# Optimization experiments

Hardware: AMD Instinct MI355X
Metric: run time of the kernel (lower is better)

Reference implementation:

```python
import jax, jax.numpy as jnp
import numpy as np

BETA = 50.0  # params['beta'] threshold for memory update
MEMORY_LEN = 4096


def setup_inputs() -> dict:
    key = jax.random.key(0)
    ks = jax.random.split(key, 7)
    B, D_IN, D_OUT, M = 256, 128, 256, MEMORY_LEN
    return {
        "x": jax.random.normal(ks[0], (B, D_IN), dtype=jnp.float32),
        "mean": jax.random.normal(ks[1], (D_IN,), dtype=jnp.float32),
        "std": jax.random.uniform(ks[2], (D_IN,), dtype=jnp.float32),
        "W1": jax.random.normal(ks[3], (D_IN, D_OUT), dtype=jnp.float32) * 0.1,
        "b1": jax.random.normal(ks[4], (D_OUT,), dtype=jnp.float32) * 0.1,
        "memory": jax.random.normal(ks[5], (M, D_OUT), dtype=jnp.float32),
        "mem_data": jax.random.normal(ks[6], (M, D_IN), dtype=jnp.float32),
    }


def reference(x, mean, std, W1, b1, memory, mem_data):
    # normalize, zeroing columns where std == 0 (as in torch forward)
    zero_std = std == 0
    denom = jnp.where(zero_std, 1.0, std)
    new = jnp.where(zero_std[None, :], 0.0, (x - mean) / denom)  # [B, D_in]

    # encoder: Linear + Tanh
    enc = jnp.tanh(new @ W1 + b1)  # [B, D_out]

    # L1 cdist against full memory (count == memory_len, steady state) + row min
    dist = jnp.abs(enc[:, None, :] - memory[None, :, :]).sum(-1)  # [B, M]
    loss = dist.min(axis=1)  # [B]

    # sequential per-row circular-buffer scatter update (side effect in torch)
    M = memory.shape[0]

    def step(carry, inp):
        mem, md, count = carry
        l, e, xi = inp
        cond = jnp.isfinite(l) & (l <= BETA)
        pos = jnp.mod(count, M)
        mem = mem.at[pos].set(jnp.where(cond, e, mem[pos]))
        md = md.at[pos].set(jnp.where(cond, xi, md[pos]))
        return (mem, md, count + cond.astype(jnp.int32)), None

    # count starts at memory_len (memory full), so writes wrap from position 0
    (mem_out, md_out, _), _ = jax.lax.scan(
        step, (memory, mem_data, jnp.int32(M)), (loss, enc, x)
    )
    return loss, mem_out, md_out
```

## Files before the change

### kernel.cpp

```cpp
#include <hip/hip_runtime.h>
#include <hip/hip_bf16.h>
#include <math.h>

#define B_ROWS 256
#define D_IN   128
#define D_OUT  256
#define M_LEN  4096
#define BETA   50.0f

#define OFF_MEM  (B_ROWS)
#define OFF_MD   (B_ROWS + M_LEN * D_OUT)

__global__ __launch_bounds__(256) void k_prep(
    const float* __restrict__ x, const float* __restrict__ mean,
    const float* __restrict__ stdv, const float* __restrict__ W1,
    const float* __restrict__ b1, float* __restrict__ enc,
    float* __restrict__ out) {
  __shared__ float sx[D_IN];
  const int b = blockIdx.x, j = threadIdx.x;
  if (j < D_IN) {
    float s = stdv[j];
    sx[j] = (s == 0.0f) ? 0.0f : (x[b * D_IN + j] - mean[j]) / s;
  }
  __syncthreads();
  float acc = b1[j];
#pragma unroll 8
  for (int k = 0; k < D_IN; ++k) acc = fmaf(sx[k], W1[k * D_OUT + j], acc);
  enc[b * D_OUT + j] = tanhf(acc);
  if (b == 0) ((unsigned int*)out)[j] = 0x7F800000u;
}

#define TB 32
#define TM 64

__global__ __launch_bounds__(256) void k_dist(
    const float* __restrict__ enc, const float* __restrict__ mem,
    const float4* __restrict__ mem4, const float4* __restrict__ md4,
    float* __restrict__ out) {
  __shared__ __align__(16) float sE[4][32][TB];
  __shared__ __align__(16) float sM[4][32][TM];

  const int t  = threadIdx.x;
  const int w  = t >> 6;
  const int l  = t & 63;
  const int ro = l >> 3;
  const int q  = l & 7;
  const int m0 = blockIdx.x * TM;
  const int b0 = blockIdx.y * TB;
  const int bid = blockIdx.y * 64 + blockIdx.x;

  const float* encp = enc + (b0 + ro) * D_OUT + w * 64 + q * 4;
  const float* memp = mem + (m0 + ro) * D_OUT + w * 64 + q * 4;

  float4 rE[4], rM[8], rE2[4], rM2[8];
  float acc[4][8] = {};

  auto store_lds = [&](const float4* e, const float4* m) {
#pragma unroll
    for (int i = 0; i < 4; ++i) {
      const int row = (i * 8 + ro) ^ (q * 4);
      sE[w][q * 4 + 0][row] = e[i].x;
      sE[w][q * 4 + 1][row] = e[i].y;
      sE[w][q * 4 + 2][row] = e[i].z;
      sE[w][q * 4 + 3][row] = e[i].w;
    }
#pragma unroll
    for (int i = 0; i < 8; ++i) {
      const int row = (i * 8 + ro) ^ (q * 4);
      sM[w][q * 4 + 0][row] = m[i].x;
      sM[w][q * 4 + 1][row] = m[i].y;
      sM[w][q * 4 + 2][row] = m[i].z;
      sM[w][q * 4 + 3][row] = m[i].w;
    }
  };

  auto compute = [&]() {
#pragma unroll
    for (int kk = 0; kk < 32; ++kk) {
      const int sw = (kk >> 2) * 4;
      float4 a   = *(const float4*)&sE[w][kk][(ro * 4) ^ sw];
      float4 bv1 = *(const float4*)&sM[w][kk][(q * 8) ^ sw];
      float4 bv2 = *(const float4*)&sM[w][kk][(q * 8 + 4) ^ sw];
      float av[4] = {a.x, a.y, a.z, a.w};
      float bw[8] = {bv1.x, bv1.y, bv1.z, bv1.w, bv2.x, bv2.y, bv2.z, bv2.w};
#pragma unroll
      for (int i = 0; i < 4; ++i)
#pragma unroll
        for (int j = 0; j < 8; ++j)
          acc[i][j] += fabsf(av[i] - bw[j]);
    }
  };

#pragma unroll
  for (int i = 0; i < 4; ++i) rE[i] = *(const float4*)(encp + i * 8 * D_OUT);
#pragma unroll
  for (int i = 0; i < 8; ++i) rM[i] = *(const float4*)(memp + i * 8 * D_OUT);
  store_lds(rE, rM);

#pragma unroll
  for (int i = 0; i < 4; ++i) rE2[i] = *(const float4*)(encp + 32 + i * 8 * D_OUT);
#pragma unroll
  for (int i = 0; i < 8; ++i) rM2[i] = *(const float4*)(memp + 32 + i * 8 * D_OUT);

  float4 cm0 = mem4[bid * 512 + t];
  float4 cm1 = mem4[bid * 512 + 256 + t];
  float4 cd0 = md4[bid * 256 + t];

  compute();
  store_lds(rE2, rM2);
  compute();

  float* sf = &sM[0][0][0];
#pragma unroll
  for (int i = 0; i < 4; ++i)
#pragma unroll
    for (int j = 0; j < 8; ++j) {
      const int p = i * 8 + j;
      sf[w * 2048 + l * 32 + (p ^ (l & 31))] = acc[i][j];
    }
  __syncthreads();

  {
    const int r = t >> 3, cg = t & 7;
    const int lv = (r >> 2) * 8 + cg;
    float dmin = 3.4e38f;
#pragma unroll
    for (int j = 0; j < 8; ++j) {
      const int p = (r & 3) * 8 + j;
      float s = sf[0 * 2048 + lv * 32 + (p ^ (lv & 31))];
      s += sf[1 * 2048 + lv * 32 + (p ^ (lv & 31))];
      s += sf[2 * 2048 + lv * 32 + (p ^ (lv & 31))];
      s += sf[3 * 2048 + lv * 32 + (p ^ (lv & 31))];
      dmin = fminf(dmin, s);
    }
    dmin = fminf(dmin, __shfl_xor(dmin, 1));
    dmin = fminf(dmin, __shfl_xor(dmin, 2));
    dmin = fminf(dmin, __shfl_xor(dmin, 4));
    if (cg == 0)
      atomicMin((unsigned int*)out + (b0 + r), __float_as_uint(dmin));
  }

  float4* mo = (float4*)(out + OFF_MEM);
  float4* dd = (float4*)(out + OFF_MD);
  mo[bid * 512 + t] = cm0;
  mo[bid * 512 + 256 + t] = cm1;
  dd[bid * 256 + t] = cd0;
}

__global__ __launch_bounds__(256) void k_scatter(float* __restrict__ out,
                                                 const float* __restrict__ enc,
                                                 const float* __restrict__ x) {
  __shared__ int wcount[4];
  int t = threadIdx.x;
  float l = out[t];
  bool cond = isfinite(l) && (l <= BETA);
  unsigned long long m = __ballot(cond);
  int lane = t & 63;
  int wv   = t >> 6;
  int pre_in_wave = __popcll(m & ((1ull << lane) - 1ull));
  if (lane == 0) wcount[wv] = (int)__popcll(m);
  __syncthreads();
  int base = 0;
  for (int w = 0; w < wv; ++w) base += wcount[w];
  if (cond) {
    int pos = base + pre_in_wave;
    float* mrow = out + OFF_MEM + pos * D_OUT;
    const float* erow = enc + t * D_OUT;
    for (int d = 0; d < D_OUT; ++d) mrow[d] = erow[d];
    float* drow = out + OFF_MD + pos * D_IN;
    const float* xrow = x + t * D_IN;
    for (int d = 0; d < D_IN; ++d) drow[d] = xrow[d];
  }
}

extern "C" void kernel_launch(void* const* d_in, const int* in_sizes, int n_in,
                              void* d_out, int out_size, void* d_ws, size_t ws_size,
                              hipStream_t stream) {
  const float* x      = (const float*)d_in[0];
  const float* mean   = (const float*)d_in[1];
  const float* stdv   = (const float*)d_in[2];
  const float* W1     = (const float*)d_in[3];
  const float* b1     = (const float*)d_in[4];
  const float* memory = (const float*)d_in[5];
  const float* memdat = (const float*)d_in[6];
  float* out = (float*)d_out;
  float* enc = (float*)d_ws;

  k_prep<<<dim3(B_ROWS), dim3(256), 0, stream>>>(x, mean, stdv, W1, b1, enc, out);

  k_dist<<<dim3(M_LEN / TM, B_ROWS / TB), dim3(256), 0, stream>>>(
      enc, memory, (const float4*)memory, (const float4*)memdat, out);

  k_scatter<<<dim3(1), dim3(256), 0, stream>>>(out, enc, x);
}
```

Measured before the change: 27.31 us.

## Fuse scatter into distance kernel via last-block completion counter

Removes the separate single-block scatter kernel launch. The last distance block to finish, found with an atomic counter in workspace that the prep kernel resets, runs the ballot/prefix-sum scatter. The change also reduces compute loop unrolling from full to 8. It adds a threadfence and atomic per block, and the scatter copy still runs serially per thread inside one block.

```diff
diff --git a/kernel.cpp b/kernel.cpp
--- a/kernel.cpp
+++ b/kernel.cpp
@@ -11,12 +11,16 @@
 #define OFF_MEM  (B_ROWS)
 #define OFF_MD   (B_ROWS + M_LEN * D_OUT)
 
+#define ENC_F   0
+#define FLAG_F  65536
+
 __global__ __launch_bounds__(256) void k_prep(
     const float* __restrict__ x, const float* __restrict__ mean,
     const float* __restrict__ stdv, const float* __restrict__ W1,
-    const float* __restrict__ b1, float* __restrict__ enc,
+    const float* __restrict__ b1, float* __restrict__ ws,
     float* __restrict__ out) {
   __shared__ float sx[D_IN];
+  float* enc = ws + ENC_F;
   const int b = blockIdx.x, j = threadIdx.x;
   if (j < D_IN) {
     float s = stdv[j];
@@ -28,17 +32,23 @@
   for (int k = 0; k < D_IN; ++k) acc = fmaf(sx[k], W1[k * D_OUT + j], acc);
   enc[b * D_OUT + j] = tanhf(acc);
   if (b == 0) ((unsigned int*)out)[j] = 0x7F800000u;
+  if (b == 0 && j == 0) ((int*)(ws + FLAG_F))[0] = 0;
 }
 
 #define TB 32
 #define TM 64
 
 __global__ __launch_bounds__(256) void k_dist(
-    const float* __restrict__ enc, const float* __restrict__ mem,
+    const float* __restrict__ x, const float* __restrict__ mem,
     const float4* __restrict__ mem4, const float4* __restrict__ md4,
-    float* __restrict__ out) {
+    float* __restrict__ ws, float* __restrict__ out) {
   __shared__ __align__(16) float sE[4][32][TB];
   __shared__ __align__(16) float sM[4][32][TM];
+  __shared__ int wcount[4];
+  __shared__ int slast;
+
+  float* enc = ws + ENC_F;
+  int*   don = (int*)(ws + FLAG_F);
 
   const int t  = threadIdx.x;
   const int w  = t >> 6;
@@ -75,7 +85,7 @@
   };
 
   auto compute = [&]() {
-#pragma unroll
+#pragma unroll 8
     for (int kk = 0; kk < 32; ++kk) {
       const int sw = (kk >> 2) * 4;
       float4 a   = *(const float4*)&sE[w][kk][(ro * 4) ^ sw];
@@ -145,31 +155,39 @@
   mo[bid * 512 + t] = cm0;
   mo[bid * 512 + 256 + t] = cm1;
   dd[bid * 256 + t] = cd0;
-}
-
-__global__ __launch_bounds__(256) void k_scatter(float* __restrict__ out,
-                                                 const float* __restrict__ enc,
-                                                 const float* __restrict__ x) {
-  __shared__ int wcount[4];
-  int t = threadIdx.x;
-  float l = out[t];
-  bool cond = isfinite(l) && (l <= BETA);
-  unsigned long long m = __ballot(cond);
-  int lane = t & 63;
-  int wv   = t >> 6;
-  int pre_in_wave = __popcll(m & ((1ull << lane) - 1ull));
-  if (lane == 0) wcount[wv] = (int)__popcll(m);
-  __syncthreads();
-  int base = 0;
-  for (int w = 0; w < wv; ++w) base += wcount[w];
-  if (cond) {
-    int pos = base + pre_in_wave;
-    float* mrow = out + OFF_MEM + pos * D_OUT;
-    const float* erow = enc + t * D_OUT;
-    for (int d = 0; d < D_OUT; ++d) mrow[d] = erow[d];
-    float* drow = out + OFF_MD + pos * D_IN;
-    const float* xrow = x + t * D_IN;
-    for (int d = 0; d < D_IN; ++d) drow[d] = xrow[d];
+
+  __threadfence();
+  __syncthreads();
+  if (t == 0) {
+    int old = __hip_atomic_fetch_add(don, 1, __ATOMIC_ACQ_REL,
+                                     __HIP_MEMORY_SCOPE_AGENT);
+    slast = (old == 511) ? 1 : 0;
+  }
+  __syncthreads();
+  if (!slast) return;
+
+  {
+    unsigned int lu = __hip_atomic_load((unsigned int*)out + t,
+                                        __ATOMIC_RELAXED,
+                                        __HIP_MEMORY_SCOPE_AGENT);
+    float mn = __uint_as_float(lu);
+    bool cond = isfinite(mn) && (mn <= BETA);
+    unsigned long long bm = __ballot(cond);
+    int lane = t & 63, wv = t >> 6;
+    int pre = __popcll(bm & ((1ull << lane) - 1ull));
+    if (lane == 0) wcount[wv] = (int)__popcll(bm);
+    __syncthreads();
+    int base = 0;
+    for (int wj = 0; wj < wv; ++wj) base += wcount[wj];
+    if (cond) {
+      int pos = base + pre;
+      float* mrow = out + OFF_MEM + pos * D_OUT;
+      const float* erow = enc + t * D_OUT;
+      for (int d = 0; d < D_OUT; ++d) mrow[d] = erow[d];
+      float* drow = out + OFF_MD + pos * D_IN;
+      const float* xrow = x + t * D_IN;
+      for (int d = 0; d < D_IN; ++d) drow[d] = xrow[d];
+    }
   }
 }
 
@@ -184,12 +202,10 @@
   const float* memory = (const float*)d_in[5];
   const float* memdat = (const float*)d_in[6];
   float* out = (float*)d_out;
-  float* enc = (float*)d_ws;
-
-  k_prep<<<dim3(B_ROWS), dim3(256), 0, stream>>>(x, mean, stdv, W1, b1, enc, out);
+  float* ws  = (float*)d_ws;
+
+  k_prep<<<dim3(B_ROWS), dim3(256), 0, stream>>>(x, mean, stdv, W1, b1, ws, out);
 
   k_dist<<<dim3(M_LEN / TM, B_ROWS / TB), dim3(256), 0, stream>>>(
-      enc, memory, (const float4*)memory, (const float4*)memdat, out);
-
-  k_scatter<<<dim3(1), dim3(256), 0, stream>>>(out, enc, x);
+      x, memory, (const float4*)memory, (const float4*)memdat, ws, out);
 }
```

Result: slower. 80.33 us (+194.1%).

## Enlarge distance tile to 64x64 with 8x8 per-thread register blocking

Applied to the files above, without the earlier changes.

The L1 distance kernel tile grows from 32 batch rows x 64 memory rows to 64x64. Each thread now accumulates an 8x8 block instead of 4x8, which raises arithmetic per LDS load and halves the number of times memory rows are reloaded across the batch dimension. The grid shrinks to 256 blocks, and each block copies twice as much memory/mem_data into the output. The costs are higher register pressure (64 accumulators), a larger LDS footprint, and fewer blocks to spread across CUs.

```diff
diff --git a/kernel.cpp b/kernel.cpp
--- a/kernel.cpp
+++ b/kernel.cpp
@@ -30,121 +30,123 @@
   if (b == 0) ((unsigned int*)out)[j] = 0x7F800000u;
 }
 
-#define TB 32
-#define TM 64
-
 __global__ __launch_bounds__(256) void k_dist(
     const float* __restrict__ enc, const float* __restrict__ mem,
     const float4* __restrict__ mem4, const float4* __restrict__ md4,
     float* __restrict__ out) {
-  __shared__ __align__(16) float sE[4][32][TB];
-  __shared__ __align__(16) float sM[4][32][TM];
+  __shared__ __align__(16) float sf[16384];
 
   const int t  = threadIdx.x;
   const int w  = t >> 6;
   const int l  = t & 63;
-  const int ro = l >> 3;
-  const int q  = l & 7;
-  const int m0 = blockIdx.x * TM;
-  const int b0 = blockIdx.y * TB;
+  const int lr = l >> 3;
+  const int lk = l & 7;
+  const int m0 = blockIdx.x * 64;
+  const int b0 = blockIdx.y * 64;
   const int bid = blockIdx.y * 64 + blockIdx.x;
 
-  const float* encp = enc + (b0 + ro) * D_OUT + w * 64 + q * 4;
-  const float* memp = mem + (m0 + ro) * D_OUT + w * 64 + q * 4;
+  const int eb = w * 4096;
+  const int mb = w * 4096 + 2048;
 
-  float4 rE[4], rM[8], rE2[4], rM2[8];
-  float acc[4][8] = {};
+  float acc[8][8] = {};
+  float4 gE[8], gM[8];
 
-  auto store_lds = [&](const float4* e, const float4* m) {
-#pragma unroll
-    for (int i = 0; i < 4; ++i) {
-      const int row = (i * 8 + ro) ^ (q * 4);
-      sE[w][q * 4 + 0][row] = e[i].x;
-      sE[w][q * 4 + 1][row] = e[i].y;
-      sE[w][q * 4 + 2][row] = e[i].z;
-      sE[w][q * 4 + 3][row] = e[i].w;
-    }
-#pragma unroll
-    for (int i = 0; i < 8; ++i) {
-      const int row = (i * 8 + ro) ^ (q * 4);
-      sM[w][q * 4 + 0][row] = m[i].x;
-      sM[w][q * 4 + 1][row] = m[i].y;
-      sM[w][q * 4 + 2][row] = m[i].z;
-      sM[w][q * 4 + 3][row] = m[i].w;
-    }
-  };
+  const float* ep = enc + (b0 + lr) * D_OUT + 64 * w + lk * 4;
+  const float* mp = mem + (m0 + lr) * D_OUT + 64 * w + lk * 4;
 
-  auto compute = [&]() {
-#pragma unroll
-    for (int kk = 0; kk < 32; ++kk) {
-      const int sw = (kk >> 2) * 4;
-      float4 a   = *(const float4*)&sE[w][kk][(ro * 4) ^ sw];
-      float4 bv1 = *(const float4*)&sM[w][kk][(q * 8) ^ sw];
-      float4 bv2 = *(const float4*)&sM[w][kk][(q * 8 + 4) ^ sw];
-      float av[4] = {a.x, a.y, a.z, a.w};
-      float bw[8] = {bv1.x, bv1.y, bv1.z, bv1.w, bv2.x, bv2.y, bv2.z, bv2.w};
-#pragma unroll
-      for (int i = 0; i < 4; ++i)
-#pragma unroll
-        for (int j = 0; j < 8; ++j)
-          acc[i][j] += fabsf(av[i] - bw[j]);
-    }
-  };
+#define LOADC(c_)                                                       \
+  do {                                                                  \
+    _Pragma("unroll")                                                   \
+    for (int i = 0; i < 8; ++i) {                                       \
+      gE[i] = *(const float4*)(ep + 32 * (c_) + i * 8 * D_OUT);         \
+      gM[i] = *(const float4*)(mp + 32 * (c_) + i * 8 * D_OUT);         \
+    }                                                                   \
+  } while (0)
+
+#define STOREC()                                                        \
+  do {                                                                  \
+    _Pragma("unroll")                                                   \
+    for (int i = 0; i < 8; ++i) {                                       \
+      const int rw = (lr + 8 * i) ^ (lk << 3);                          \
+      const int be = eb + lk * 256 + rw;                                \
+      sf[be] = gE[i].x;       sf[be + 64] = gE[i].y;                    \
+      sf[be + 128] = gE[i].z; sf[be + 192] = gE[i].w;                   \
+      const int bm = mb + lk * 256 + rw;                                \
+      sf[bm] = gM[i].x;       sf[bm + 64] = gM[i].y;                    \
+      sf[bm + 128] = gM[i].z; sf[bm + 192] = gM[i].w;                   \
+    }                                                                   \
+  } while (0)
+
+#define COMPUTEC()                                                      \
+  do {                                                                  \
+    for (int g = 0; g < 8; ++g) {                                       \
+      const int es = eb + g * 256 + ((lr ^ g) << 3);                    \
+      const int ms = mb + g * 256 + ((lk ^ g) << 3);                    \
+      _Pragma("unroll")                                                 \
+      for (int j2 = 0; j2 < 4; ++j2) {                                  \
+        float4 e0 = *(const float4*)&sf[es + j2 * 64];                  \
+        float4 e1 = *(const float4*)&sf[es + j2 * 64 + 4];              \
+        float4 v0 = *(const float4*)&sf[ms + j2 * 64];                  \
+        float4 v1 = *(const float4*)&sf[ms + j2 * 64 + 4];              \
+        float av[8] = {e0.x, e0.y, e0.z, e0.w, e1.x, e1.y, e1.z, e1.w}; \
+        float bw[8] = {v0.x, v0.y, v0.z, v0.w, v1.x, v1.y, v1.z, v1.w}; \
+        _Pragma("unroll")                                               \
+        for (int i = 0; i < 8; ++i)                                     \
+          _Pragma("unroll")                                             \
+          for (int j = 0; j < 8; ++j)                                   \
+            acc[i][j] += fabsf(av[i] - bw[j]);                          \
+      }                                                                 \
+    }                                                                   \
+  } while (0)
+
+  LOADC(0);
+  STOREC();
+  LOADC(1);
+  COMPUTEC();
+  STOREC();
+  float4 cm0 = mem4[bid * 1024 + t];
+  float4 cm1 = mem4[bid * 1024 + 256 + t];
+  float4 cm2 = mem4[bid * 1024 + 512 + t];
+  float4 cm3 = mem4[bid * 1024 + 768 + t];
+  float4 cd0 = md4[bid * 512 + t];
+  float4 cd1 = md4[bid * 512 + 256 + t];
+  COMPUTEC();
 
 #pragma unroll
-  for (int i = 0; i < 4; ++i) rE[i] = *(const float4*)(encp + i * 8 * D_OUT);
-#pragma unroll
-  for (int i = 0; i < 8; ++i) rM[i] = *(const float4*)(memp + i * 8 * D_OUT);
-  store_lds(rE, rM);
-
-#pragma unroll
-  for (int i = 0; i < 4; ++i) rE2[i] = *(const float4*)(encp + 32 + i * 8 * D_OUT);
-#pragma unroll
-  for (int i = 0; i < 8; ++i) rM2[i] = *(const float4*)(memp + 32 + i * 8 * D_OUT);
-
-  float4 cm0 = mem4[bid * 512 + t];
-  float4 cm1 = mem4[bid * 512 + 256 + t];
-  float4 cd0 = md4[bid * 256 + t];
-
-  compute();
-  store_lds(rE2, rM2);
-  compute();
-
-  float* sf = &sM[0][0][0];
-#pragma unroll
-  for (int i = 0; i < 4; ++i)
+  for (int i = 0; i < 8; ++i)
 #pragma unroll
     for (int j = 0; j < 8; ++j) {
       const int p = i * 8 + j;
-      sf[w * 2048 + l * 32 + (p ^ (l & 31))] = acc[i][j];
+      sf[w * 4096 + l * 64 + (p ^ l)] = acc[i][j];
     }
   __syncthreads();
 
   {
-    const int r = t >> 3, cg = t & 7;
-    const int lv = (r >> 2) * 8 + cg;
+    const int r = t >> 2, cg = t & 3;
     float dmin = 3.4e38f;
 #pragma unroll
-    for (int j = 0; j < 8; ++j) {
-      const int p = (r & 3) * 8 + j;
-      float s = sf[0 * 2048 + lv * 32 + (p ^ (lv & 31))];
-      s += sf[1 * 2048 + lv * 32 + (p ^ (lv & 31))];
-      s += sf[2 * 2048 + lv * 32 + (p ^ (lv & 31))];
-      s += sf[3 * 2048 + lv * 32 + (p ^ (lv & 31))];
+    for (int cc = 0; cc < 16; ++cc) {
+      const int c = cg * 16 + cc;
+      const int ll = (r >> 3) * 8 + (c >> 3);
+      const int p = (r & 7) * 8 + (c & 7);
+      const int off = ll * 64 + (p ^ ll);
+      float s = sf[off] + sf[4096 + off] + sf[8192 + off] + sf[12288 + off];
       dmin = fminf(dmin, s);
     }
     dmin = fminf(dmin, __shfl_xor(dmin, 1));
     dmin = fminf(dmin, __shfl_xor(dmin, 2));
-    dmin = fminf(dmin, __shfl_xor(dmin, 4));
     if (cg == 0)
       atomicMin((unsigned int*)out + (b0 + r), __float_as_uint(dmin));
   }
 
   float4* mo = (float4*)(out + OFF_MEM);
   float4* dd = (float4*)(out + OFF_MD);
-  mo[bid * 512 + t] = cm0;
-  mo[bid * 512 + 256 + t] = cm1;
-  dd[bid * 256 + t] = cd0;
+  mo[bid * 1024 + t] = cm0;
+  mo[bid * 1024 + 256 + t] = cm1;
+  mo[bid * 1024 + 512 + t] = cm2;
+  mo[bid * 1024 + 768 + t] = cm3;
+  dd[bid * 512 + t] = cd0;
+  dd[bid * 512 + 256 + t] = cd1;
 }
 
 __global__ __launch_bounds__(256) void k_scatter(float* __restrict__ out,
@@ -188,7 +190,7 @@
 
   k_prep<<<dim3(B_ROWS), dim3(256), 0, stream>>>(x, mean, stdv, W1, b1, enc, out);
 
-  k_dist<<<dim3(M_LEN / TM, B_ROWS / TB), dim3(256), 0, stream>>>(
+  k_dist<<<dim3(M_LEN / 64, B_ROWS / 64), dim3(256), 0, stream>>>(
       enc, memory, (const float4*)memory, (const float4*)memdat, out);
 
   k_scatter<<<dim3(1), dim3(256), 0, stream>>>(out, enc, x);
```

New measurement: 36.66 us. 34.2% more time.
